# Kernel tuning notes

Measured on AMD Instinct MI355X. Metric: run time of the kernel, lower is better.

## Reference

```python
import jax, jax.numpy as jnp
import numpy as np

N_STATE = 64   # S4 state size N
L_MAX = 4096   # sequence length
H = 256        # number of SSM channels (d_model)
BATCH = 16


def _green_roots(Lambda, P, B, C, step, L):
    """Frequency-domain S4 kernel at the L roots of unity (Q = P, DPLR).
    Lambda,P,B,C: complex[N]; step: scalar. Returns complex[L]."""
    Omega = jnp.exp(-2j * jnp.pi * (jnp.arange(L) / L))          # (L,)
    g = (2.0 / step) * ((1.0 - Omega) / (1.0 + Omega))           # (L,)
    c = 2.0 / (1.0 + Omega)                                      # (L,)
    # four Cauchy numerators stacked: k00,k01,k10,k11
    vs = jnp.stack([C.conj() * B, C.conj() * P,
                    P.conj() * B, P.conj() * P])                 # (4,N)
    denom = g[:, None] - Lambda[None, :]                         # (L,N)
    k = jnp.einsum('kn,ln->kl', vs, 1.0 / denom)                 # (4,L)
    k00, k01, k10, k11 = k
    return c * (k00 - k01 * (1.0 / (1.0 + k11)) * k10)           # (L,)


def _kernel_freq(Lambda_re, Lambda_im, P_re, P_im, B_re, B_im,
                 C_re, C_im, log_step, L):
    Lambda = (Lambda_re + 1j * Lambda_im).astype(jnp.complex64)  # (H,N)
    P = (P_re + 1j * P_im).astype(jnp.complex64)
    Bm = (B_re + 1j * B_im).astype(jnp.complex64)
    Cm = (C_re + 1j * C_im).astype(jnp.complex64)
    step = jnp.exp(log_step)                                     # (H,)
    f = lambda lam, p, b, c, s: _green_roots(lam, p, b, c, s, L)
    return jax.vmap(f)(Lambda, P, Bm, Cm, step)                  # (H,L)


def setup_inputs() -> dict:
    key = jax.random.key(0)
    ks = jax.random.split(key, 10)
    u = jax.random.normal(ks[0], (BATCH, H, L_MAX), dtype=jnp.float32)
    # stable continuous-time poles: negative real part, spread imag parts
    Lambda_re = -0.5 * jnp.ones((H, N_STATE), jnp.float32) \
        - jax.random.uniform(ks[1], (H, N_STATE), dtype=jnp.float32)
    Lambda_im = jnp.pi * jax.random.normal(ks[2], (H, N_STATE), dtype=jnp.float32) * N_STATE / 8
    scale = 1.0 / np.sqrt(N_STATE)
    P_re = scale * jax.random.normal(ks[3], (H, N_STATE), dtype=jnp.float32)
    P_im = scale * jax.random.normal(ks[4], (H, N_STATE), dtype=jnp.float32)
    B_re = scale * jax.random.normal(ks[5], (H, N_STATE), dtype=jnp.float32)
    B_im = scale * jax.random.normal(ks[6], (H, N_STATE), dtype=jnp.float32)
    C_re = scale * jax.random.normal(ks[7], (H, N_STATE), dtype=jnp.float32)
    C_im = scale * jax.random.normal(ks[8], (H, N_STATE), dtype=jnp.float32)
    # log-uniform step in [1e-3, 1e-1] (log_step_initializer)
    log_step = (jax.random.uniform(ks[9], (H,), dtype=jnp.float32)
                * (np.log(0.1) - np.log(0.001)) + np.log(0.001)).astype(jnp.float32)
    return {"u": u, "Lambda_re": Lambda_re, "Lambda_im": Lambda_im,
            "P_re": P_re, "P_im": P_im, "B_re": B_re, "B_im": B_im,
            "C_re": C_re, "C_im": C_im, "log_step": log_step}


def reference(u, Lambda_re, Lambda_im, P_re, P_im, B_re, B_im,
              C_re, C_im, log_step):
    L = u.shape[-1]
    Kf = _kernel_freq(Lambda_re, Lambda_im, P_re, P_im, B_re, B_im,
                      C_re, C_im, log_step, L)                   # (H,L) complex
    # circular_convolution_complex, batched over (BATCH,H)
    ud = jnp.fft.fft(u, axis=-1)                                  # (B,H,L)
    y = jnp.fft.ifft(ud * Kf[None, :, :], n=L, axis=-1)
    return y.real.astype(jnp.float32)                             # (B,H,L)
```

## Files before the change

kernel.cpp:

```cpp
#include <hip/hip_runtime.h>
#include <math.h>

#define NSTATE 64
#define LEN    4096
#define NH     256
#define NB     16

__device__ float2 g_ksym[NH * LEN];
__device__ float4 g_pA[NH * NSTATE];
__device__ float4 g_pB[NH * NSTATE];
__device__ float2 g_pC[NH * NSTATE];

__device__ __forceinline__ int rev8_12(int p) {
  return ((p & 7) << 9) | (((p >> 3) & 7) << 6) | (((p >> 6) & 7) << 3) | (p >> 9);
}

__device__ __forceinline__ float2 cadd(float2 a, float2 b){ return make_float2(a.x+b.x, a.y+b.y); }
__device__ __forceinline__ float2 csub(float2 a, float2 b){ return make_float2(a.x-b.x, a.y-b.y); }
__device__ __forceinline__ float2 cmul(float2 a, float2 b){ return make_float2(a.x*b.x - a.y*b.y, a.x*b.y + a.y*b.x); }
__device__ __forceinline__ float2 mulnegi(float2 a){ return make_float2(a.y, -a.x); }
__device__ __forceinline__ float2 mulposi(float2 a){ return make_float2(-a.y, a.x); }

#define RSQ2 0.70710678118654752f

__device__ __forceinline__ void bfly8_fwd(float2 v[8]) {
  float2 a0 = cadd(v[0], v[4]), b0 = csub(v[0], v[4]);
  float2 a1 = cadd(v[1], v[5]), d1 = csub(v[1], v[5]);
  float2 a2 = cadd(v[2], v[6]), d2 = csub(v[2], v[6]);
  float2 a3 = cadd(v[3], v[7]), d3 = csub(v[3], v[7]);
  float2 b1 = make_float2(RSQ2 * (d1.x + d1.y), RSQ2 * (d1.y - d1.x));
  float2 b2 = mulnegi(d2);
  float2 b3 = make_float2(RSQ2 * (d3.y - d3.x), -RSQ2 * (d3.x + d3.y));
  float2 u0 = cadd(a0, a2), u1 = csub(a0, a2), u2 = cadd(a1, a3), u3 = csub(a1, a3);
  v[0] = cadd(u0, u2);
  v[2] = cadd(u1, mulnegi(u3));
  v[4] = csub(u0, u2);
  v[6] = cadd(u1, mulposi(u3));
  float2 w0 = cadd(b0, b2), w1 = csub(b0, b2), w2 = cadd(b1, b3), w3 = csub(b1, b3);
  v[1] = cadd(w0, w2);
  v[3] = cadd(w1, mulnegi(w3));
  v[5] = csub(w0, w2);
  v[7] = cadd(w1, mulposi(w3));
}

__device__ __forceinline__ void bfly8_inv(float2 v[8]) {
  float2 a0 = cadd(v[0], v[4]), b0 = csub(v[0], v[4]);
  float2 a1 = cadd(v[1], v[5]), d1 = csub(v[1], v[5]);
  float2 a2 = cadd(v[2], v[6]), d2 = csub(v[2], v[6]);
  float2 a3 = cadd(v[3], v[7]), d3 = csub(v[3], v[7]);
  float2 b1 = make_float2(RSQ2 * (d1.x - d1.y), RSQ2 * (d1.x + d1.y));
  float2 b2 = mulposi(d2);
  float2 b3 = make_float2(-RSQ2 * (d3.x + d3.y), RSQ2 * (d3.x - d3.y));
  float2 u0 = cadd(a0, a2), u1 = csub(a0, a2), u2 = cadd(a1, a3), u3 = csub(a1, a3);
  v[0] = cadd(u0, u2);
  v[2] = cadd(u1, mulposi(u3));
  v[4] = csub(u0, u2);
  v[6] = cadd(u1, mulnegi(u3));
  float2 w0 = cadd(b0, b2), w1 = csub(b0, b2), w2 = cadd(b1, b3), w3 = csub(b1, b3);
  v[1] = cadd(w0, w2);
  v[3] = cadd(w1, mulposi(w3));
  v[5] = csub(w0, w2);
  v[7] = cadd(w1, mulnegi(w3));
}

__device__ __forceinline__ void twiddle7(float2 v[8], float wr, float wi) {
  float2 w1 = make_float2(wr, wi);
  float2 w2 = cmul(w1, w1);
  float2 w3 = cmul(w2, w1);
  float2 w4 = cmul(w2, w2);
  float2 w5 = cmul(w3, w2);
  float2 w6 = cmul(w3, w3);
  float2 w7 = cmul(w4, w3);
  v[1] = cmul(v[1], w1); v[2] = cmul(v[2], w2); v[3] = cmul(v[3], w3);
  v[4] = cmul(v[4], w4); v[5] = cmul(v[5], w5); v[6] = cmul(v[6], w6);
  v[7] = cmul(v[7], w7);
}

__global__ __launch_bounds__(256) void s4_prep(
    const float* __restrict__ Lre, const float* __restrict__ Lim,
    const float* __restrict__ Pre, const float* __restrict__ Pim,
    const float* __restrict__ Bre, const float* __restrict__ Bim,
    const float* __restrict__ Cre, const float* __restrict__ Cim)
{
  int idx = blockIdx.x * 256 + threadIdx.x;
  if (idx >= NH * NSTATE) return;
  float lr = Lre[idx], li = Lim[idx];
  float pr = Pre[idx], pi = Pim[idx];
  float br = Bre[idx], bi = Bim[idx];
  float cr = Cre[idx], ci = Cim[idx];
  g_pA[idx] = make_float4(lr, li, pr * pr + pi * pi, 0.0f);
  g_pB[idx] = make_float4(cr * br + ci * bi, cr * bi - ci * br,
                          cr * pr + ci * pi, cr * pi - ci * pr);
  g_pC[idx] = make_float2(pr * br + pi * bi, pr * bi - pi * br);
}

__global__ __launch_bounds__(1024) void s4_kernel_freq(const float* __restrict__ log_step)
{
  __shared__ float2 kf[LEN];
  const int h = blockIdx.x, tid = threadIdx.x;
  const float step = expf(log_step[h]);
  const float ts = 2.0f / step;
  const float NEG2PI = -6.2831853071795864769f;

  float gr[4], gi[4];
#pragma unroll
  for (int j = 0; j < 4; ++j) {
    int l = tid + 1024 * j;
    float ang = NEG2PI * ((float)l * (1.0f / (float)LEN));
    float so, co; sincosf(ang, &so, &co);
    float dr = 1.0f + co, di = so;
    float inv = 1.0f / (dr * dr + di * di);
    float nr = 1.0f - co, ni = -so;
    gr[j] = ts * ((nr * dr + ni * di) * inv);
    gi[j] = ts * ((ni * dr - nr * di) * inv);
  }

  float k00r[4] = {0,0,0,0}, k00i[4] = {0,0,0,0};
  float k01r[4] = {0,0,0,0}, k01i[4] = {0,0,0,0};
  float k10r[4] = {0,0,0,0}, k10i[4] = {0,0,0,0};
  float k11r[4] = {0,0,0,0}, k11i[4] = {0,0,0,0};

  const float4* __restrict__ pa = g_pA + h * NSTATE;
  const float4* __restrict__ pb = g_pB + h * NSTATE;
  const float2* __restrict__ pc = g_pC + h * NSTATE;

#pragma unroll 4
  for (int n = 0; n < NSTATE; ++n) {
    float4 A  = pa[n];
    float4 Bv = pb[n];
    float2 Cv = pc[n];
#pragma unroll
    for (int j = 0; j < 4; ++j) {
      float rd = gr[j] - A.x, id = gi[j] - A.y;
      float idn = __builtin_amdgcn_rcpf(fmaf(rd, rd, id * id));
      float ir = rd * idn, ii = -id * idn;
      k00r[j] += Bv.x * ir - Bv.y * ii;  k00i[j] += Bv.x * ii + Bv.y * ir;
      k01r[j] += Bv.z * ir - Bv.w * ii;  k01i[j] += Bv.z * ii + Bv.w * ir;
      k10r[j] += Cv.x * ir - Cv.y * ii;  k10i[j] += Cv.x * ii + Cv.y * ir;
      k11r[j] += A.z * ir;               k11i[j] += A.z * ii;
    }
  }

#pragma unroll
  for (int j = 0; j < 4; ++j) {
    int l = tid + 1024 * j;
    float ang = NEG2PI * ((float)l * (1.0f / (float)LEN));
    float so, co; sincosf(ang, &so, &co);
    float dr = 1.0f + co, di = so;
    float inv = 1.0f / (dr * dr + di * di);
    float c_re = 2.0f * dr * inv, c_im = -2.0f * di * inv;
    float rr = 1.0f + k11r[j], ri = k11i[j];
    float rinv = 1.0f / (rr * rr + ri * ri);
    float pr_ = k01r[j] * k10r[j] - k01i[j] * k10i[j];
    float pi_ = k01r[j] * k10i[j] + k01i[j] * k10r[j];
    float wr = (pr_ * rr + pi_ * ri) * rinv;
    float wi = (pi_ * rr - pr_ * ri) * rinv;
    float sr = k00r[j] - wr, si = k00i[j] - wi;
    int ph = l ^ ((l >> 6) & 63);
    kf[ph] = make_float2(c_re * sr - c_im * si, c_re * si + c_im * sr);
  }
  __syncthreads();

  float2* out = &g_ksym[(size_t)h * LEN];
  for (int p = tid; p < LEN; p += 1024) {
    int kk = rev8_12(p);
    int k2 = (LEN - kk) & (LEN - 1);
    float2 a = kf[kk ^ ((kk >> 6) & 63)];
    float2 b = kf[k2 ^ ((k2 >> 6) & 63)];
    out[p] = make_float2(0.5f * (a.x + b.x), 0.5f * (a.y - b.y));
  }
}

__global__ __launch_bounds__(512) void s4_fftconv(const float* __restrict__ u,
                                                 float* __restrict__ y)
{
  __shared__ float2 X[4608];

  const int t = threadIdx.x;
  const int bid = blockIdx.x;
  const int h  = bid & (NH - 1);
  const int bp = bid >> 8;

  float c1, s1, c2, s2, c3, s3;
  sincosf((float)t         * (-6.2831853071795864769f / 4096.0f), &s1, &c1);
  sincosf((float)(t & 63)  * (-6.2831853071795864769f /  512.0f), &s2, &c2);
  sincosf((float)(t & 7)   * (-6.2831853071795864769f /   64.0f), &s3, &c3);

  const float* u1 = u + ((size_t)bp * NH + h) * LEN;
  const float* u2 = u + ((size_t)(bp + 8) * NH + h) * LEN;

  float2 v[8];
#pragma unroll
  for (int m = 0; m < 8; ++m)
    v[m] = make_float2(u1[t + 512 * m], u2[t + 512 * m]);
  bfly8_fwd(v);
  twiddle7(v, c1, s1);
#pragma unroll
  for (int m = 0; m < 8; ++m) X[t + 512 * m] = v[m];
  __syncthreads();

  {
    int B = t >> 6, j = t & 63, base = B * 512 + j;
#pragma unroll
    for (int m = 0; m < 8; ++m) v[m] = X[base + 64 * m];
  }
  __syncthreads();
  bfly8_fwd(v);
  twiddle7(v, c2, s2);
  {
    int B = t >> 6, j = t & 63;
#pragma unroll
    for (int m = 0; m < 8; ++m) X[68 * (8 * B + m) + j] = v[m];
  }
  __syncthreads();

  {
    int b = t >> 3, j = t & 7;
#pragma unroll
    for (int m = 0; m < 8; ++m) v[m] = X[68 * b + j + 8 * m];
  }
  __syncthreads();
  bfly8_fwd(v);
  twiddle7(v, c3, s3);
  {
    int b = t >> 3, j = t & 7;
#pragma unroll
    for (int m = 0; m < 8; ++m) X[9 * (8 * b + m) + j] = v[m];
  }
  __syncthreads();

  {
    const float4* kp = (const float4*)(g_ksym + (size_t)h * LEN + 8 * t);
    float4 k0 = kp[0], k1 = kp[1], k2 = kp[2], k3 = kp[3];
#pragma unroll
    for (int m = 0; m < 8; ++m) v[m] = X[9 * t + m];
    bfly8_fwd(v);
    v[0] = cmul(v[0], make_float2(k0.x, k0.y));
    v[1] = cmul(v[1], make_float2(k0.z, k0.w));
    v[2] = cmul(v[2], make_float2(k1.x, k1.y));
    v[3] = cmul(v[3], make_float2(k1.z, k1.w));
    v[4] = cmul(v[4], make_float2(k2.x, k2.y));
    v[5] = cmul(v[5], make_float2(k2.z, k2.w));
    v[6] = cmul(v[6], make_float2(k3.x, k3.y));
    v[7] = cmul(v[7], make_float2(k3.z, k3.w));
    bfly8_inv(v);
#pragma unroll
    for (int p = 0; p < 8; ++p) X[9 * t + p] = v[p];
  }
  __syncthreads();

  {
    int b = t >> 3, j = t & 7;
#pragma unroll
    for (int m = 0; m < 8; ++m) v[m] = X[9 * (8 * b + m) + j];
  }
  twiddle7(v, c3, -s3);
  bfly8_inv(v);
  __syncthreads();
  {
    int b = t >> 3, j = t & 7;
#pragma unroll
    for (int p = 0; p < 8; ++p) X[68 * b + j + 8 * p] = v[p];
  }
  __syncthreads();

  {
    int B = t >> 6, j = t & 63;
#pragma unroll
    for (int m = 0; m < 8; ++m) v[m] = X[68 * (8 * B + m) + j];
  }
  twiddle7(v, c2, -s2);
  bfly8_inv(v);
  __syncthreads();
  {
    int B = t >> 6, j = t & 63, base = B * 512 + j;
#pragma unroll
    for (int p = 0; p < 8; ++p) X[base + 64 * p] = v[p];
  }
  __syncthreads();

#pragma unroll
  for (int m = 0; m < 8; ++m) v[m] = X[t + 512 * m];
  twiddle7(v, c1, -s1);
  bfly8_inv(v);

  float* y1 = y + ((size_t)bp * NH + h) * LEN;
  float* y2 = y + ((size_t)(bp + 8) * NH + h) * LEN;
  const float sc = 1.0f / (float)LEN;
#pragma unroll
  for (int p = 0; p < 8; ++p) {
    y1[t + 512 * p] = v[p].x * sc;
    y2[t + 512 * p] = v[p].y * sc;
  }
}

extern "C" void kernel_launch(void* const* d_in, const int* in_sizes, int n_in,
                              void* d_out, int out_size, void* d_ws, size_t ws_size,
                              hipStream_t stream) {
  const float* u    = (const float*)d_in[0];
  const float* Lre  = (const float*)d_in[1];
  const float* Lim  = (const float*)d_in[2];
  const float* Pre  = (const float*)d_in[3];
  const float* Pim  = (const float*)d_in[4];
  const float* Bre  = (const float*)d_in[5];
  const float* Bim  = (const float*)d_in[6];
  const float* Cre  = (const float*)d_in[7];
  const float* Cim  = (const float*)d_in[8];
  const float* lstep = (const float*)d_in[9];
  float* y = (float*)d_out;

  s4_prep<<<(NH * NSTATE + 255) / 256, 256, 0, stream>>>(Lre, Lim, Pre, Pim, Bre, Bim, Cre, Cim);
  s4_kernel_freq<<<NH, 1024, 0, stream>>>(lstep);
  s4_fftconv<<<NH * (NB / 2), 512, 0, stream>>>(u, y);
}
```

Baseline: 192.3 us.

## Exploit conjugate symmetry in Cauchy kernel evaluation and split reorder into separate kernel

Each thread now evaluates the Cauchy sums at frequency q and its conjugate partner L-q. Because the frequency-domain values at those points are conjugates, both symmetric outputs are written directly. The grid changes from 256 blocks of 1024 threads to 1024 blocks of 256 threads. The bit-reversed reordering that used shared memory moves into a new s4_reorder kernel, which costs an extra launch and a global round-trip through a new g_knat buffer.

```diff
diff --git a/kernel.cpp b/kernel.cpp
--- a/kernel.cpp
+++ b/kernel.cpp
@@ -6,6 +6,7 @@
 #define NH     256
 #define NB     16
 
+__device__ float2 g_knat[NH * LEN];
 __device__ float2 g_ksym[NH * LEN];
 __device__ float4 g_pA[NH * NSTATE];
 __device__ float4 g_pB[NH * NSTATE];
@@ -94,80 +95,132 @@
   g_pC[idx] = make_float2(pr * br + pi * bi, pr * bi - pi * br);
 }
 
-__global__ __launch_bounds__(1024) void s4_kernel_freq(const float* __restrict__ log_step)
+__global__ __launch_bounds__(256) void s4_kernel_freq(const float* __restrict__ log_step)
 {
-  __shared__ float2 kf[LEN];
-  const int h = blockIdx.x, tid = threadIdx.x;
+  const int b = blockIdx.x;
+  const int h = b >> 2;
+  const int q = ((b & 3) << 8) | threadIdx.x;
   const float step = expf(log_step[h]);
   const float ts = 2.0f / step;
   const float NEG2PI = -6.2831853071795864769f;
 
-  float gr[4], gi[4];
-#pragma unroll
-  for (int j = 0; j < 4; ++j) {
-    int l = tid + 1024 * j;
-    float ang = NEG2PI * ((float)l * (1.0f / (float)LEN));
-    float so, co; sincosf(ang, &so, &co);
+  float gar, gai, car, cai, gbr, gbi, cbr, cbi;
+  float gcr, gci, ccr, cci, gdr, gdi, cdr, cdi;
+  {
+    float so, co;
+    sincosf(NEG2PI * ((float)q * (1.0f / (float)LEN)), &so, &co);
     float dr = 1.0f + co, di = so;
-    float inv = 1.0f / (dr * dr + di * di);
+    float inv = 1.0f / fmaf(dr, dr, di * di);
+    car = 2.0f * dr * inv; cai = -2.0f * di * inv;
     float nr = 1.0f - co, ni = -so;
-    gr[j] = ts * ((nr * dr + ni * di) * inv);
-    gi[j] = ts * ((ni * dr - nr * di) * inv);
-  }
-
-  float k00r[4] = {0,0,0,0}, k00i[4] = {0,0,0,0};
-  float k01r[4] = {0,0,0,0}, k01i[4] = {0,0,0,0};
-  float k10r[4] = {0,0,0,0}, k10i[4] = {0,0,0,0};
-  float k11r[4] = {0,0,0,0}, k11i[4] = {0,0,0,0};
+    gar = ts * (fmaf(nr, dr, ni * di) * inv);
+    gai = ts * (fmaf(ni, dr, -nr * di) * inv);
+  }
+  if (q == 0) {
+    float so, co;
+    sincosf(NEG2PI * 0.5f, &so, &co);
+    float dr = 1.0f + co, di = so;
+    float inv = 1.0f / fmaf(dr, dr, di * di);
+    cbr = 2.0f * dr * inv; cbi = -2.0f * di * inv;
+    float nr = 1.0f - co, ni = -so;
+    gbr = ts * (fmaf(nr, dr, ni * di) * inv);
+    gbi = ts * (fmaf(ni, dr, -nr * di) * inv);
+  } else {
+    gbr = gar; gbi = -gai; cbr = car; cbi = -cai;
+  }
+  {
+    float so, co;
+    sincosf(NEG2PI * ((float)(q + 1024) * (1.0f / (float)LEN)), &so, &co);
+    float dr = 1.0f + co, di = so;
+    float inv = 1.0f / fmaf(dr, dr, di * di);
+    ccr = 2.0f * dr * inv; cci = -2.0f * di * inv;
+    float nr = 1.0f - co, ni = -so;
+    gcr = ts * (fmaf(nr, dr, ni * di) * inv);
+    gci = ts * (fmaf(ni, dr, -nr * di) * inv);
+  }
+  gdr = gcr; gdi = -gci; cdr = ccr; cdi = -cci;
+
+  float A00r=0,A00i=0,A01r=0,A01i=0,A10r=0,A10i=0,A11r=0,A11i=0;
+  float B00r=0,B00i=0,B01r=0,B01i=0,B10r=0,B10i=0,B11r=0,B11i=0;
+  float C00r=0,C00i=0,C01r=0,C01i=0,C10r=0,C10i=0,C11r=0,C11i=0;
+  float D00r=0,D00i=0,D01r=0,D01i=0,D10r=0,D10i=0,D11r=0,D11i=0;
 
   const float4* __restrict__ pa = g_pA + h * NSTATE;
   const float4* __restrict__ pb = g_pB + h * NSTATE;
   const float2* __restrict__ pc = g_pC + h * NSTATE;
 
+#define CAUCHY(gre, gim, k00r,k00i,k01r,k01i,k10r,k10i,k11r,k11i)            \
+  {                                                                          \
+    float rd = gre - Av.x, id = gim - Av.y;                                  \
+    float idn = __builtin_amdgcn_rcpf(fmaf(rd, rd, id * id));                \
+    float ir = rd * idn, ii = -(id * idn);                                   \
+    k00r = fmaf(Bv.x, ir, k00r); k00r = fmaf(-Bv.y, ii, k00r);               \
+    k00i = fmaf(Bv.x, ii, k00i); k00i = fmaf(Bv.y, ir, k00i);                \
+    k01r = fmaf(Bv.z, ir, k01r); k01r = fmaf(-Bv.w, ii, k01r);               \
+    k01i = fmaf(Bv.z, ii, k01i); k01i = fmaf(Bv.w, ir, k01i);                \
+    k10r = fmaf(Cv.x, ir, k10r); k10r = fmaf(-Cv.y, ii, k10r);               \
+    k10i = fmaf(Cv.x, ii, k10i); k10i = fmaf(Cv.y, ir, k10i);                \
+    k11r = fmaf(Av.z, ir, k11r); k11i = fmaf(Av.z, ii, k11i);                \
+  }
+
 #pragma unroll 4
   for (int n = 0; n < NSTATE; ++n) {
-    float4 A  = pa[n];
+    float4 Av = pa[n];
     float4 Bv = pb[n];
     float2 Cv = pc[n];
-#pragma unroll
-    for (int j = 0; j < 4; ++j) {
-      float rd = gr[j] - A.x, id = gi[j] - A.y;
-      float idn = __builtin_amdgcn_rcpf(fmaf(rd, rd, id * id));
-      float ir = rd * idn, ii = -id * idn;
-      k00r[j] += Bv.x * ir - Bv.y * ii;  k00i[j] += Bv.x * ii + Bv.y * ir;
-      k01r[j] += Bv.z * ir - Bv.w * ii;  k01i[j] += Bv.z * ii + Bv.w * ir;
-      k10r[j] += Cv.x * ir - Cv.y * ii;  k10i[j] += Cv.x * ii + Cv.y * ir;
-      k11r[j] += A.z * ir;               k11i[j] += A.z * ii;
-    }
-  }
-
-#pragma unroll
-  for (int j = 0; j < 4; ++j) {
-    int l = tid + 1024 * j;
-    float ang = NEG2PI * ((float)l * (1.0f / (float)LEN));
-    float so, co; sincosf(ang, &so, &co);
-    float dr = 1.0f + co, di = so;
-    float inv = 1.0f / (dr * dr + di * di);
-    float c_re = 2.0f * dr * inv, c_im = -2.0f * di * inv;
-    float rr = 1.0f + k11r[j], ri = k11i[j];
-    float rinv = 1.0f / (rr * rr + ri * ri);
-    float pr_ = k01r[j] * k10r[j] - k01i[j] * k10i[j];
-    float pi_ = k01r[j] * k10i[j] + k01i[j] * k10r[j];
-    float wr = (pr_ * rr + pi_ * ri) * rinv;
-    float wi = (pi_ * rr - pr_ * ri) * rinv;
-    float sr = k00r[j] - wr, si = k00i[j] - wi;
-    int ph = l ^ ((l >> 6) & 63);
-    kf[ph] = make_float2(c_re * sr - c_im * si, c_re * si + c_im * sr);
-  }
-  __syncthreads();
-
-  float2* out = &g_ksym[(size_t)h * LEN];
-  for (int p = tid; p < LEN; p += 1024) {
-    int kk = rev8_12(p);
-    int k2 = (LEN - kk) & (LEN - 1);
-    float2 a = kf[kk ^ ((kk >> 6) & 63)];
-    float2 b = kf[k2 ^ ((k2 >> 6) & 63)];
-    out[p] = make_float2(0.5f * (a.x + b.x), 0.5f * (a.y - b.y));
+    CAUCHY(gar, gai, A00r,A00i,A01r,A01i,A10r,A10i,A11r,A11i)
+    CAUCHY(gbr, gbi, B00r,B00i,B01r,B01i,B10r,B10i,B11r,B11i)
+    CAUCHY(gcr, gci, C00r,C00i,C01r,C01i,C10r,C10i,C11r,C11i)
+    CAUCHY(gdr, gdi, D00r,D00i,D01r,D01i,D10r,D10i,D11r,D11i)
+  }
+#undef CAUCHY
+
+#define FINISH(cr_, ci_, k00r,k00i,k01r,k01i,k10r,k10i,k11r,k11i, Kr, Ki)    \
+  {                                                                          \
+    float rr = 1.0f + k11r, ri = k11i;                                       \
+    float rinv = 1.0f / fmaf(rr, rr, ri * ri);                               \
+    float pr_ = k01r * k10r - k01i * k10i;                                   \
+    float pi_ = k01r * k10i + k01i * k10r;                                   \
+    float wr = (pr_ * rr + pi_ * ri) * rinv;                                 \
+    float wi = (pi_ * rr - pr_ * ri) * rinv;                                 \
+    float sr = k00r - wr, si = k00i - wi;                                    \
+    Kr = cr_ * sr - ci_ * si; Ki = cr_ * si + ci_ * sr;                      \
+  }
+
+  float Kar, Kai, Kbr, Kbi, Kcr, Kci, Kdr, Kdi;
+  FINISH(car, cai, A00r,A00i,A01r,A01i,A10r,A10i,A11r,A11i, Kar, Kai)
+  FINISH(cbr, cbi, B00r,B00i,B01r,B01i,B10r,B10i,B11r,B11i, Kbr, Kbi)
+  FINISH(ccr, cci, C00r,C00i,C01r,C01i,C10r,C10i,C11r,C11i, Kcr, Kci)
+  FINISH(cdr, cdi, D00r,D00i,D01r,D01i,D10r,D10i,D11r,D11i, Kdr, Kdi)
+#undef FINISH
+
+  float2* out = g_knat + (size_t)h * LEN;
+  if (q == 0) {
+    out[0]    = make_float2(Kar, 0.0f);
+    out[2048] = make_float2(Kbr, 0.0f);
+  } else {
+    float fr = 0.5f * (Kar + Kbr), fi = 0.5f * (Kai - Kbi);
+    out[q]        = make_float2(fr, fi);
+    out[LEN - q]  = make_float2(fr, -fi);
+  }
+  {
+    float fr = 0.5f * (Kcr + Kdr), fi = 0.5f * (Kci - Kdi);
+    out[1024 + q] = make_float2(fr, fi);
+    out[3072 - q] = make_float2(fr, -fi);
+  }
+}
+
+__global__ __launch_bounds__(256) void s4_reorder()
+{
+  __shared__ float2 s[LEN];
+  const int h = blockIdx.x, t = threadIdx.x;
+  const float2* __restrict__ in = g_knat + (size_t)h * LEN;
+  float2* __restrict__ out = g_ksym + (size_t)h * LEN;
+  for (int i = t; i < LEN; i += 256) s[i ^ ((i >> 6) & 63)] = in[i];
+  __syncthreads();
+  for (int p = t; p < LEN; p += 256) {
+    int l = rev8_12(p);
+    out[p] = s[l ^ ((l >> 6) & 63)];
   }
 }
 
@@ -310,6 +363,7 @@
   float* y = (float*)d_out;
 
   s4_prep<<<(NH * NSTATE + 255) / 256, 256, 0, stream>>>(Lre, Lim, Pre, Pim, Bre, Bim, Cre, Cim);
-  s4_kernel_freq<<<NH, 1024, 0, stream>>>(lstep);
+  s4_kernel_freq<<<NH * 4, 256, 0, stream>>>(lstep);
+  s4_reorder<<<NH, 256, 0, stream>>>();
   s4_fftconv<<<NH * (NB / 2), 512, 0, stream>>>(u, y);
 }
```

Result: faster. 184.6 us (-4.0%).
